# Optimization experiments

Measured on AMD Instinct MI355X. Metric: run time of the kernel, lower is better.

## Reference

```python
import jax, jax.numpy as jnp
import numpy as np

B, C_IN, H, W = 8, 112, 16, 16
D = 128            # patch_embed_dim
N_BANK = 200000
CHUNK = 1024       # query_chunk_size
NN_K = 3
TOPK_RATIO = 0.03  # reduction = 'topk_mean'


def setup_inputs() -> dict:
    key = jax.random.key(0)
    k1, k2, k3 = jax.random.split(key, 3)
    feature_map = jax.random.normal(k1, (B, C_IN, H, W), dtype=jnp.float32)
    proj_w = jax.random.normal(k2, (D, C_IN), dtype=jnp.float32) * 0.05
    memory_bank = jax.random.normal(k3, (N_BANK, D), dtype=jnp.float32)
    return {"feature_map": feature_map, "proj_w": proj_w, "memory_bank": memory_bank}


def _l2norm(x, axis=-1, eps=1e-12):
    return x / jnp.maximum(jnp.linalg.norm(x, axis=axis, keepdims=True), eps)


def reference(feature_map, proj_w, memory_bank):
    b, c, h, w = feature_map.shape
    patches = h * w
    # patch embeddings: NHWC flatten -> linear proj (no bias) -> L2 normalize
    emb = feature_map.transpose(0, 2, 3, 1).reshape(-1, c)        # [Q, C_in]
    emb = _l2norm(emb @ proj_w.T)                                  # [Q, D]
    bank = _l2norm(memory_bank)                                    # [N, D]
    bank_t = bank.T                                                # [D, N]

    q_total = emb.shape[0]
    n_chunks = q_total // CHUNK if q_total % CHUNK == 0 else -(-q_total // CHUNK)
    pad = n_chunks * CHUNK - q_total
    emb_p = jnp.pad(emb, ((0, pad), (0, 0)))
    chunks = emb_p.reshape(n_chunks, CHUNK, -1)

    def chunk_fn(q):                                               # q: [CHUNK, D]
        sims = q @ bank_t                                          # [CHUNK, N]
        best_sim, _ = jax.lax.top_k(sims, NN_K)                    # [CHUNK, k]
        dist = jnp.sqrt(jnp.maximum(2.0 - 2.0 * best_sim, 0.0))
        return dist.mean(axis=1)                                   # [CHUNK]

    patch_d = jax.lax.map(chunk_fn, chunks).reshape(-1)[:q_total]
    patch_d = patch_d.reshape(b, patches)                          # [B, P]

    # topk_mean reduction over patches
    k = min(patches, max(1, int(np.ceil(patches * TOPK_RATIO))))
    top_vals, _ = jax.lax.top_k(patch_d, k)
    return top_vals.mean(axis=1)                                   # [B]
```

## Files before the change

### kernel.cpp

```cpp
#include <hip/hip_runtime.h>
#include <stdint.h>

#define N_BANK 200000
#define N_PAD  201600
#define NQ     2048
#define DIMD   128
#define C_IN   112
#define NCHUNK 63
#define CHUNK_COLS 3200
#define NSTEP  25
#define NCE    126
#define NC3    378

typedef short v8s __attribute__((ext_vector_type(8)));
typedef float v4f __attribute__((ext_vector_type(4)));

typedef const __attribute__((address_space(1))) uint32_t* gp1_t;
typedef __attribute__((address_space(3))) uint32_t* lp3_t;

__device__ __forceinline__ void async16(const void* g, void* l) {
  __builtin_amdgcn_global_load_lds((gp1_t)g, (lp3_t)l, 16, 0, 0);
}

__device__ __forceinline__ unsigned short f2bf(float f) {
  uint32_t u = __float_as_uint(f);
  u += 0x7fff + ((u >> 16) & 1);
  return (unsigned short)(u >> 16);
}

__device__ __forceinline__ void insert3(float& m1, float& m2, float& m3, float v) {
  m3 = __builtin_amdgcn_fmed3f(m2, m3, v);
  m2 = __builtin_amdgcn_fmed3f(m1, m2, v);
  m1 = fmaxf(m1, v);
}

__global__ void emb_kernel(const float* __restrict__ fm, const float* __restrict__ pw,
                           unsigned short* __restrict__ embB) {
  int q = blockIdx.x;
  int b = q >> 8, p = q & 255;
  int tid = threadIdx.x;
  __shared__ float x[C_IN];
  __shared__ float wsum[2];
  if (tid < C_IN) x[tid] = fm[(b * C_IN + tid) * 256 + p];
  __syncthreads();
  const float* row = pw + tid * C_IN;
  float dot = 0.f;
#pragma unroll
  for (int c = 0; c < C_IN; ++c) dot = fmaf(x[c], row[c], dot);
  float s = dot * dot;
#pragma unroll
  for (int off = 32; off; off >>= 1) s += __shfl_xor(s, off);
  int lane = tid & 63, wv = tid >> 6;
  if (lane == 0) wsum[wv] = s;
  __syncthreads();
  float ss = wsum[0] + wsum[1];
  float scale = 1.f / fmaxf(sqrtf(ss), 1e-12f);
  int j = tid >> 3, pos = tid & 7;
  int sw = j ^ (q & 15);
  embB[q * DIMD + sw * 8 + pos] = f2bf(dot * scale);
}

__global__ void bank_kernel(const float* __restrict__ bank, unsigned short* __restrict__ bankB) {
  int tid = threadIdx.x;
  int wv = tid >> 6, lane = tid & 63;
  int r = blockIdx.x * 4 + wv;
  if (r >= N_PAD) return;
  uint32_t* out = (uint32_t*)bankB;
  int j = lane >> 2, w = lane & 3;
  int sdw = ((j ^ (r & 15)) << 2) | w;
  if (r < N_BANK) {
    float2 v = ((const float2*)bank)[r * 64 + lane];
    float s = v.x * v.x + v.y * v.y;
#pragma unroll
    for (int off = 32; off; off >>= 1) s += __shfl_xor(s, off);
    float scale = 1.f / fmaxf(sqrtf(s), 1e-12f);
    uint32_t lo = f2bf(v.x * scale);
    uint32_t hi = f2bf(v.y * scale);
    out[r * 64 + sdw] = lo | (hi << 16);
  } else {
    out[r * 64 + sdw] = 0u;
  }
}

__global__ __launch_bounds__(256, 2)
void sim_top3_kernel(const unsigned short* __restrict__ embB,
                     const unsigned short* __restrict__ bankB,
                     float* __restrict__ partial) {
  int mt = blockIdx.x;
  int chunk = blockIdx.y;
  int q0 = mt * 128;
  int tid = threadIdx.x;
  int wv = tid >> 6, lane = tid & 63;
  int wr = wv >> 1, wc = wv & 1;
  int g = lane >> 4, c0 = lane & 15;

  __shared__ __align__(16) unsigned char lds[32768];

  {
    const char* gbase = (const char*)embB + q0 * 256;
#pragma unroll
    for (int i = 0; i < 8; ++i) {
      int off = (wv * 8 + i) * 1024 + lane * 16;
      async16(gbase + off, lds + off);
    }
  }
  __syncthreads();

  v8s a[4][4];
#pragma unroll
  for (int fm = 0; fm < 4; ++fm)
#pragma unroll
    for (int k = 0; k < 4; ++k) {
      int row = wr * 64 + fm * 16 + c0;
      a[fm][k] = *(const v8s*)(lds + row * 256 + (((k * 4 + g) ^ c0) << 4));
    }

  float m1[16], m2[16], m3[16];
#pragma unroll
  for (int t = 0; t < 16; ++t) { m1[t] = -1e30f; m2[t] = -1e30f; m3[t] = -1e30f; }

  const char* bbase = (const char*)bankB + (size_t)chunk * CHUNK_COLS * 256;
  for (int s = 0; s < NSTEP; ++s) {
    __syncthreads();
#pragma unroll
    for (int i = 0; i < 8; ++i) {
      int off = (wv * 8 + i) * 1024 + lane * 16;
      async16(bbase + (size_t)s * 128 * 256 + off, lds + off);
    }
    __syncthreads();

#pragma unroll
    for (int fn = 0; fn < 4; ++fn) {
      v8s bf[4];
      int col = wc * 64 + fn * 16 + c0;
#pragma unroll
      for (int k = 0; k < 4; ++k)
        bf[k] = *(const v8s*)(lds + col * 256 + (((k * 4 + g) ^ c0) << 4));
#pragma unroll
      for (int fm = 0; fm < 4; ++fm) {
        v4f acc = {0.f, 0.f, 0.f, 0.f};
#pragma unroll
        for (int k = 0; k < 4; ++k)
          acc = __builtin_amdgcn_mfma_f32_16x16x32_bf16(a[fm][k], bf[k], acc, 0, 0, 0);
#pragma unroll
        for (int j = 0; j < 4; ++j)
          insert3(m1[fm * 4 + j], m2[fm * 4 + j], m3[fm * 4 + j], acc[j]);
      }
    }
  }

#pragma unroll
  for (int mask = 1; mask < 16; mask <<= 1) {
#pragma unroll
    for (int t = 0; t < 16; ++t) {
      float b1 = __shfl_xor(m1[t], mask);
      float b2 = __shfl_xor(m2[t], mask);
      float b3 = __shfl_xor(m3[t], mask);
      insert3(m1[t], m2[t], m3[t], b1);
      insert3(m1[t], m2[t], m3[t], b2);
      insert3(m1[t], m2[t], m3[t], b3);
    }
  }

  if (c0 == 0) {
    int ce = chunk * 2 + wc;
#pragma unroll
    for (int t = 0; t < 16; ++t) {
      int q = q0 + wr * 64 + (t >> 2) * 16 + g * 4 + (t & 3);
      float* dst = partial + (size_t)q * NC3 + ce * 3;
      dst[0] = m1[t];
      dst[1] = m2[t];
      dst[2] = m3[t];
    }
  }
}

__global__ void merge1_kernel(const float* __restrict__ partial, float* __restrict__ pd) {
  int q = (blockIdx.x * blockDim.x + threadIdx.x) >> 6;
  int lane = threadIdx.x & 63;
  const float* src = partial + (size_t)q * NC3;
  float m1 = -1e30f, m2 = -1e30f, m3 = -1e30f;
  for (int c = lane; c < NC3; c += 64) insert3(m1, m2, m3, src[c]);
#pragma unroll
  for (int mask = 32; mask; mask >>= 1) {
    float b1 = __shfl_xor(m1, mask);
    float b2 = __shfl_xor(m2, mask);
    float b3 = __shfl_xor(m3, mask);
    insert3(m1, m2, m3, b1);
    insert3(m1, m2, m3, b2);
    insert3(m1, m2, m3, b3);
  }
  if (lane == 0) {
    float d1 = sqrtf(fmaxf(2.f - 2.f * m1, 0.f));
    float d2 = sqrtf(fmaxf(2.f - 2.f * m2, 0.f));
    float d3 = sqrtf(fmaxf(2.f - 2.f * m3, 0.f));
    pd[q] = (d1 + d2 + d3) * (1.f / 3.f);
  }
}

__global__ void merge2_kernel(const float* __restrict__ pd, float* __restrict__ out) {
  int b = blockIdx.x;
  int tid = threadIdx.x;
  __shared__ float vals[256];
  __shared__ float rv[256];
  __shared__ int ri[256];
  vals[tid] = pd[b * 256 + tid];
  __syncthreads();
  float sum = 0.f;
  for (int iter = 0; iter < 8; ++iter) {
    rv[tid] = vals[tid]; ri[tid] = tid;
    __syncthreads();
    for (int s = 128; s > 0; s >>= 1) {
      if (tid < s && rv[tid + s] > rv[tid]) { rv[tid] = rv[tid + s]; ri[tid] = ri[tid + s]; }
      __syncthreads();
    }
    sum += rv[0];
    if (tid == 0) vals[ri[0]] = -1e30f;
    __syncthreads();
  }
  if (tid == 0) out[b] = sum * (1.f / 8.f);
}

extern "C" void kernel_launch(void* const* d_in, const int* in_sizes, int n_in,
                              void* d_out, int out_size, void* d_ws, size_t ws_size,
                              hipStream_t stream) {
  const float* fm   = (const float*)d_in[0];
  const float* pw   = (const float*)d_in[1];
  const float* bank = (const float*)d_in[2];
  float* out = (float*)d_out;

  char* ws = (char*)d_ws;
  unsigned short* bankB = (unsigned short*)ws;
  unsigned short* embB  = (unsigned short*)(ws + 51609600);
  float* partial        = (float*)(ws + 51609600 + 524288);
  float* pd             = (float*)(ws + 51609600 + 524288 + 3096576);

  emb_kernel<<<NQ, 128, 0, stream>>>(fm, pw, embB);
  bank_kernel<<<N_PAD / 4, 256, 0, stream>>>(bank, bankB);
  sim_top3_kernel<<<dim3(16, NCHUNK), 256, 0, stream>>>(embB, bankB, partial);
  merge1_kernel<<<NQ / 4, 256, 0, stream>>>(partial, pd);
  merge2_kernel<<<8, 256, 0, stream>>>(pd, out);
}
```

Measured before the change: 309.3 us.

## Load MFMA operands directly from global memory, dropping LDS staging and swizzle

The similarity kernel no longer stages query and bank tiles through LDS with barriers. Each lane now reads its bf16 MFMA fragments straight from global memory, relying on L2/L1 for reuse, and the XOR swizzle is removed from the emb and bank layouts. The bank normalization kernel becomes a grid-stride loop over 1024 blocks. This removes the barriers and LDS traffic but gives up explicit tile sharing between waves, adds redundant global loads, and leaves little latency hiding inside the step loop.

```diff
diff --git a/kernel.cpp b/kernel.cpp
--- a/kernel.cpp
+++ b/kernel.cpp
@@ -15,13 +15,6 @@
 typedef short v8s __attribute__((ext_vector_type(8)));
 typedef float v4f __attribute__((ext_vector_type(4)));
 
-typedef const __attribute__((address_space(1))) uint32_t* gp1_t;
-typedef __attribute__((address_space(3))) uint32_t* lp3_t;
-
-__device__ __forceinline__ void async16(const void* g, void* l) {
-  __builtin_amdgcn_global_load_lds((gp1_t)g, (lp3_t)l, 16, 0, 0);
-}
-
 __device__ __forceinline__ unsigned short f2bf(float f) {
   uint32_t u = __float_as_uint(f);
   u += 0x7fff + ((u >> 16) & 1);
@@ -55,30 +48,26 @@
   __syncthreads();
   float ss = wsum[0] + wsum[1];
   float scale = 1.f / fmaxf(sqrtf(ss), 1e-12f);
-  int j = tid >> 3, pos = tid & 7;
-  int sw = j ^ (q & 15);
-  embB[q * DIMD + sw * 8 + pos] = f2bf(dot * scale);
+  embB[q * DIMD + tid] = f2bf(dot * scale);
 }
 
 __global__ void bank_kernel(const float* __restrict__ bank, unsigned short* __restrict__ bankB) {
   int tid = threadIdx.x;
   int wv = tid >> 6, lane = tid & 63;
-  int r = blockIdx.x * 4 + wv;
-  if (r >= N_PAD) return;
   uint32_t* out = (uint32_t*)bankB;
-  int j = lane >> 2, w = lane & 3;
-  int sdw = ((j ^ (r & 15)) << 2) | w;
-  if (r < N_BANK) {
-    float2 v = ((const float2*)bank)[r * 64 + lane];
-    float s = v.x * v.x + v.y * v.y;
-#pragma unroll
-    for (int off = 32; off; off >>= 1) s += __shfl_xor(s, off);
-    float scale = 1.f / fmaxf(sqrtf(s), 1e-12f);
-    uint32_t lo = f2bf(v.x * scale);
-    uint32_t hi = f2bf(v.y * scale);
-    out[r * 64 + sdw] = lo | (hi << 16);
-  } else {
-    out[r * 64 + sdw] = 0u;
+  for (int r = blockIdx.x * 4 + wv; r < N_PAD; r += gridDim.x * 4) {
+    if (r < N_BANK) {
+      float2 v = ((const float2*)bank)[r * 64 + lane];
+      float s = v.x * v.x + v.y * v.y;
+#pragma unroll
+      for (int off = 32; off; off >>= 1) s += __shfl_xor(s, off);
+      float scale = 1.f / fmaxf(sqrtf(s), 1e-12f);
+      uint32_t lo = f2bf(v.x * scale);
+      uint32_t hi = f2bf(v.y * scale);
+      out[r * 64 + lane] = lo | (hi << 16);
+    } else {
+      out[r * 64 + lane] = 0u;
+    }
   }
 }
 
@@ -94,54 +83,37 @@
   int wr = wv >> 1, wc = wv & 1;
   int g = lane >> 4, c0 = lane & 15;
 
-  __shared__ __align__(16) unsigned char lds[32768];
-
-  {
-    const char* gbase = (const char*)embB + q0 * 256;
-#pragma unroll
-    for (int i = 0; i < 8; ++i) {
-      int off = (wv * 8 + i) * 1024 + lane * 16;
-      async16(gbase + off, lds + off);
-    }
-  }
-  __syncthreads();
-
+  const char* arow = (const char*)embB + (size_t)(q0 + wr * 64 + c0) * 256 + g * 16;
   v8s a[4][4];
 #pragma unroll
   for (int fm = 0; fm < 4; ++fm)
 #pragma unroll
-    for (int k = 0; k < 4; ++k) {
-      int row = wr * 64 + fm * 16 + c0;
-      a[fm][k] = *(const v8s*)(lds + row * 256 + (((k * 4 + g) ^ c0) << 4));
-    }
+    for (int k = 0; k < 4; ++k)
+      a[fm][k] = *(const v8s*)(arow + fm * 16 * 256 + k * 64);
 
   float m1[16], m2[16], m3[16];
 #pragma unroll
   for (int t = 0; t < 16; ++t) { m1[t] = -1e30f; m2[t] = -1e30f; m3[t] = -1e30f; }
 
-  const char* bbase = (const char*)bankB + (size_t)chunk * CHUNK_COLS * 256;
+  const char* bbase = (const char*)bankB
+                    + ((size_t)chunk * CHUNK_COLS + wc * 64 + c0) * 256 + g * 16;
   for (int s = 0; s < NSTEP; ++s) {
-    __syncthreads();
-#pragma unroll
-    for (int i = 0; i < 8; ++i) {
-      int off = (wv * 8 + i) * 1024 + lane * 16;
-      async16(bbase + (size_t)s * 128 * 256 + off, lds + off);
-    }
-    __syncthreads();
+    const char* bs = bbase + (size_t)s * 128 * 256;
+    v8s bf[4][4];
+#pragma unroll
+    for (int fn = 0; fn < 4; ++fn)
+#pragma unroll
+      for (int k = 0; k < 4; ++k)
+        bf[fn][k] = *(const v8s*)(bs + fn * 16 * 256 + k * 64);
 
 #pragma unroll
     for (int fn = 0; fn < 4; ++fn) {
-      v8s bf[4];
-      int col = wc * 64 + fn * 16 + c0;
-#pragma unroll
-      for (int k = 0; k < 4; ++k)
-        bf[k] = *(const v8s*)(lds + col * 256 + (((k * 4 + g) ^ c0) << 4));
 #pragma unroll
       for (int fm = 0; fm < 4; ++fm) {
         v4f acc = {0.f, 0.f, 0.f, 0.f};
 #pragma unroll
         for (int k = 0; k < 4; ++k)
-          acc = __builtin_amdgcn_mfma_f32_16x16x32_bf16(a[fm][k], bf[k], acc, 0, 0, 0);
+          acc = __builtin_amdgcn_mfma_f32_16x16x32_bf16(a[fm][k], bf[fn][k], acc, 0, 0, 0);
 #pragma unroll
         for (int j = 0; j < 4; ++j)
           insert3(m1[fm * 4 + j], m2[fm * 4 + j], m3[fm * 4 + j], acc[j]);
@@ -236,7 +208,7 @@
   float* pd             = (float*)(ws + 51609600 + 524288 + 3096576);
 
   emb_kernel<<<NQ, 128, 0, stream>>>(fm, pw, embB);
-  bank_kernel<<<N_PAD / 4, 256, 0, stream>>>(bank, bankB);
+  bank_kernel<<<1024, 256, 0, stream>>>(bank, bankB);
   sim_top3_kernel<<<dim3(16, NCHUNK), 256, 0, stream>>>(embB, bankB, partial);
   merge1_kernel<<<NQ / 4, 256, 0, stream>>>(partial, pd);
   merge2_kernel<<<8, 256, 0, stream>>>(pd, out);
```

After: 404.7 us. 1.31x slower.

## Widen sim tile to 256 queries per block, load A directly, grid-stride bank prep

Applied to the files above, without the earlier changes.

The similarity kernel now gives each wave its own 64 query rows and has it sweep all 128 bank columns of each LDS tile. Each block therefore covers 256 queries, which halves the number of blocks that reload the whole bank through LDS. Query fragments are read straight from global memory in an unswizzled layout, so the initial LDS stage and its barrier are gone. The partial top-3 buffer shrinks to one entry per chunk, occupancy is requested at 3 blocks per CU, and the bank normalization kernel switches to a fixed 1024-block grid-stride loop. In exchange, fewer blocks are launched (504), which may underfill the GPU, and register pressure rises.

```diff
diff --git a/kernel.cpp b/kernel.cpp
--- a/kernel.cpp
+++ b/kernel.cpp
@@ -9,8 +9,7 @@
 #define NCHUNK 63
 #define CHUNK_COLS 3200
 #define NSTEP  25
-#define NCE    126
-#define NC3    378
+#define NC3    189
 
 typedef short v8s __attribute__((ext_vector_type(8)));
 typedef float v4f __attribute__((ext_vector_type(4)));
@@ -55,65 +54,51 @@
   __syncthreads();
   float ss = wsum[0] + wsum[1];
   float scale = 1.f / fmaxf(sqrtf(ss), 1e-12f);
-  int j = tid >> 3, pos = tid & 7;
-  int sw = j ^ (q & 15);
-  embB[q * DIMD + sw * 8 + pos] = f2bf(dot * scale);
+  embB[q * DIMD + tid] = f2bf(dot * scale);
 }
 
 __global__ void bank_kernel(const float* __restrict__ bank, unsigned short* __restrict__ bankB) {
   int tid = threadIdx.x;
   int wv = tid >> 6, lane = tid & 63;
-  int r = blockIdx.x * 4 + wv;
-  if (r >= N_PAD) return;
   uint32_t* out = (uint32_t*)bankB;
   int j = lane >> 2, w = lane & 3;
-  int sdw = ((j ^ (r & 15)) << 2) | w;
-  if (r < N_BANK) {
-    float2 v = ((const float2*)bank)[r * 64 + lane];
-    float s = v.x * v.x + v.y * v.y;
-#pragma unroll
-    for (int off = 32; off; off >>= 1) s += __shfl_xor(s, off);
-    float scale = 1.f / fmaxf(sqrtf(s), 1e-12f);
-    uint32_t lo = f2bf(v.x * scale);
-    uint32_t hi = f2bf(v.y * scale);
-    out[r * 64 + sdw] = lo | (hi << 16);
-  } else {
-    out[r * 64 + sdw] = 0u;
-  }
-}
-
-__global__ __launch_bounds__(256, 2)
+  for (int r = blockIdx.x * 4 + wv; r < N_PAD; r += gridDim.x * 4) {
+    int sdw = ((j ^ (r & 15)) << 2) | w;
+    if (r < N_BANK) {
+      float2 v = ((const float2*)bank)[r * 64 + lane];
+      float s = v.x * v.x + v.y * v.y;
+#pragma unroll
+      for (int off = 32; off; off >>= 1) s += __shfl_xor(s, off);
+      float scale = 1.f / fmaxf(sqrtf(s), 1e-12f);
+      uint32_t lo = f2bf(v.x * scale);
+      uint32_t hi = f2bf(v.y * scale);
+      out[r * 64 + sdw] = lo | (hi << 16);
+    } else {
+      out[r * 64 + sdw] = 0u;
+    }
+  }
+}
+
+__global__ __launch_bounds__(256, 3)
 void sim_top3_kernel(const unsigned short* __restrict__ embB,
                      const unsigned short* __restrict__ bankB,
                      float* __restrict__ partial) {
   int mt = blockIdx.x;
   int chunk = blockIdx.y;
-  int q0 = mt * 128;
+  int q0 = mt * 256;
   int tid = threadIdx.x;
   int wv = tid >> 6, lane = tid & 63;
-  int wr = wv >> 1, wc = wv & 1;
   int g = lane >> 4, c0 = lane & 15;
 
   __shared__ __align__(16) unsigned char lds[32768];
 
-  {
-    const char* gbase = (const char*)embB + q0 * 256;
-#pragma unroll
-    for (int i = 0; i < 8; ++i) {
-      int off = (wv * 8 + i) * 1024 + lane * 16;
-      async16(gbase + off, lds + off);
-    }
-  }
-  __syncthreads();
-
+  const char* arow = (const char*)embB + (size_t)(q0 + wv * 64 + c0) * 256 + g * 16;
   v8s a[4][4];
 #pragma unroll
   for (int fm = 0; fm < 4; ++fm)
 #pragma unroll
-    for (int k = 0; k < 4; ++k) {
-      int row = wr * 64 + fm * 16 + c0;
-      a[fm][k] = *(const v8s*)(lds + row * 256 + (((k * 4 + g) ^ c0) << 4));
-    }
+    for (int k = 0; k < 4; ++k)
+      a[fm][k] = *(const v8s*)(arow + fm * 16 * 256 + k * 64);
 
   float m1[16], m2[16], m3[16];
 #pragma unroll
@@ -130,9 +115,9 @@
     __syncthreads();
 
 #pragma unroll
-    for (int fn = 0; fn < 4; ++fn) {
+    for (int fn = 0; fn < 8; ++fn) {
       v8s bf[4];
-      int col = wc * 64 + fn * 16 + c0;
+      int col = fn * 16 + c0;
 #pragma unroll
       for (int k = 0; k < 4; ++k)
         bf[k] = *(const v8s*)(lds + col * 256 + (((k * 4 + g) ^ c0) << 4));
@@ -163,11 +148,10 @@
   }
 
   if (c0 == 0) {
-    int ce = chunk * 2 + wc;
 #pragma unroll
     for (int t = 0; t < 16; ++t) {
-      int q = q0 + wr * 64 + (t >> 2) * 16 + g * 4 + (t & 3);
-      float* dst = partial + (size_t)q * NC3 + ce * 3;
+      int q = q0 + wv * 64 + (t >> 2) * 16 + g * 4 + (t & 3);
+      float* dst = partial + (size_t)q * NC3 + chunk * 3;
       dst[0] = m1[t];
       dst[1] = m2[t];
       dst[2] = m3[t];
@@ -233,11 +217,11 @@
   unsigned short* bankB = (unsigned short*)ws;
   unsigned short* embB  = (unsigned short*)(ws + 51609600);
   float* partial        = (float*)(ws + 51609600 + 524288);
-  float* pd             = (float*)(ws + 51609600 + 524288 + 3096576);
+  float* pd             = (float*)(ws + 51609600 + 524288 + 1548288);
 
   emb_kernel<<<NQ, 128, 0, stream>>>(fm, pw, embB);
-  bank_kernel<<<N_PAD / 4, 256, 0, stream>>>(bank, bankB);
-  sim_top3_kernel<<<dim3(16, NCHUNK), 256, 0, stream>>>(embB, bankB, partial);
+  bank_kernel<<<1024, 256, 0, stream>>>(bank, bankB);
+  sim_top3_kernel<<<dim3(8, NCHUNK), 256, 0, stream>>>(embB, bankB, partial);
   merge1_kernel<<<NQ / 4, 256, 0, stream>>>(partial, pd);
   merge2_kernel<<<8, 256, 0, stream>>>(pd, out);
 }
```

Measured after the change: 329.1 us. 6.4% more time.
